# Kernel optimization log

Hardware: AMD Instinct MI355X
Metric: run time of the kernel (lower is better)

Reference implementation:

```python
import jax, jax.numpy as jnp
import numpy as np

N, E, H, R = 16384, 262144, 256, 64
INV_SQRT_3 = 1.0 / np.sqrt(3.0)
INV_SQRT_H = 1.0 / np.sqrt(float(H))
INV_SQRT_2 = 1.0 / np.sqrt(2.0)


def ssilu(t):
    # ScaledSiLU: silu(x) / 0.6
    return jax.nn.silu(t) * (1.0 / 0.6)


def layernorm(x, g, b):
    m = jnp.mean(x, axis=-1, keepdims=True)
    v = jnp.var(x, axis=-1, keepdims=True)
    return (x - m) * jax.lax.rsqrt(v + 1e-5) * g + b


def gated_equivariant_block(x, v, Wv1, Wv2, Wu1, bu1, Wu2, bu2, out_ch):
    # x: [N, Cin], v: [N, 3, Cin]
    vec1 = jnp.linalg.norm(v @ Wv1, axis=-2)          # [N, Cin]
    vec2 = v @ Wv2                                     # [N, 3, out_ch]
    h = ssilu(jnp.concatenate([x, vec1], axis=-1) @ Wu1 + bu1) @ Wu2 + bu2
    xn, vn = h[..., :out_ch], h[..., out_ch:]
    return ssilu(xn), vn[:, None, :] * vec2


def setup_inputs() -> dict:
    key = jax.random.key(0)
    ks = iter(jax.random.split(key, 48))

    def w(shape, fan_in):
        return jax.random.normal(next(ks), shape, jnp.float32) / np.sqrt(float(fan_in))

    return {
        "x": jax.random.normal(next(ks), (N, H), jnp.float32),
        "vec": jax.random.normal(next(ks), (N, 3, H), jnp.float32),
        "edge_rbf": jax.random.uniform(next(ks), (E, R), jnp.float32),
        "edge_vector": jax.random.normal(next(ks), (E, 3), jnp.float32),
        # PaiNNMessage params
        "ln_g": jnp.ones((H,), jnp.float32), "ln_b": jnp.zeros((H,), jnp.float32),
        "W_x1": w((H, H), H), "b_x1": jnp.zeros((H,), jnp.float32),
        "W_x2": w((H, 3 * H), H), "b_x2": jnp.zeros((3 * H,), jnp.float32),
        "W_rbf": w((R, 3 * H), R), "b_rbf": jnp.zeros((3 * H,), jnp.float32),
        # PaiNNUpdate params
        "W_vp": w((H, 2 * H), H),
        "W_xv1": w((2 * H, H), 2 * H), "b_xv1": jnp.zeros((H,), jnp.float32),
        "W_xv2": w((H, 3 * H), H), "b_xv2": jnp.zeros((3 * H,), jnp.float32),
        # PaiNNOutput block 1 (H -> H//2)
        "o1_Wv1": w((H, H), H), "o1_Wv2": w((H, H // 2), H),
        "o1_Wu1": w((2 * H, H), 2 * H), "o1_bu1": jnp.zeros((H,), jnp.float32),
        "o1_Wu2": w((H, H), H), "o1_bu2": jnp.zeros((H,), jnp.float32),
        # PaiNNOutput block 2 (H//2 -> 1)
        "o2_Wv1": w((H // 2, H // 2), H // 2), "o2_Wv2": w((H // 2, 1), H // 2),
        "o2_Wu1": w((H, H // 2), H), "o2_bu1": jnp.zeros((H // 2,), jnp.float32),
        "o2_Wu2": w((H // 2, 2), H // 2), "o2_bu2": jnp.zeros((2,), jnp.float32),
        "edge_index": jax.random.randint(next(ks), (2, E), 0, N),
    }


def reference(x, vec, edge_rbf, edge_vector,
              ln_g, ln_b, W_x1, b_x1, W_x2, b_x2, W_rbf, b_rbf,
              W_vp, W_xv1, b_xv1, W_xv2, b_xv2,
              o1_Wv1, o1_Wv2, o1_Wu1, o1_bu1, o1_Wu2, o1_bu2,
              o2_Wv1, o2_Wv2, o2_Wu1, o2_bu1, o2_Wu2, o2_bu2,
              edge_index):
    src, dst = edge_index[0], edge_index[1]

    # ---- PaiNNMessage ----
    xh = ssilu(layernorm(x, ln_g, ln_b) @ W_x1 + b_x1) @ W_x2 + b_x2   # [N, 3H]
    rbfh = edge_rbf @ W_rbf + b_rbf                                     # [E, 3H]
    m = xh[src] * rbfh                                                  # gather + fuse
    m1, m2, m3 = m[:, :H], m[:, H:2 * H], m[:, 2 * H:]
    m2 = m2 * INV_SQRT_3
    vmsg = (vec[src] * m2[:, None, :] + m3[:, None, :] * edge_vector[:, :, None]) * INV_SQRT_H  # [E,3,H]
    dx = jax.ops.segment_sum(m1, dst, num_segments=N)
    dvec = jax.ops.segment_sum(vmsg, dst, num_segments=N)
    x = x + dx
    vec = vec + dvec

    # ---- PaiNNUpdate ----
    vp = vec @ W_vp                                    # [N, 3, 2H]
    vec1, vec2 = vp[..., :H], vp[..., H:]
    vec_dot = jnp.sum(vec1 * vec2, axis=1) * INV_SQRT_H            # [N, H]
    vnorm = jnp.sqrt(jnp.sum(vec2 * vec2, axis=-2) + 1e-8)          # [N, H]
    xvh = ssilu(jnp.concatenate([x, vnorm], axis=-1) @ W_xv1 + b_xv1) @ W_xv2 + b_xv2
    xv1, xv2, xv3 = xvh[:, :H], xvh[:, H:2 * H], xvh[:, 2 * H:]
    x = x + (xv1 + xv2 * vec_dot) * INV_SQRT_2
    vec = vec + xv3[:, None, :] * vec1

    # ---- PaiNNOutput ----
    x, vec = gated_equivariant_block(x, vec, o1_Wv1, o1_Wv2, o1_Wu1, o1_bu1, o1_Wu2, o1_bu2, H // 2)
    x, vec = gated_equivariant_block(x, vec, o2_Wv1, o2_Wv2, o2_Wu1, o2_bu1, o2_Wu2, o2_bu2, 1)
    return jnp.squeeze(vec, axis=-1)   # [N, 3]
```

## Files before the change

### kernel.cpp

```cpp
#include <hip/hip_runtime.h>
#include <math.h>

#define NN 16384
#define EE 262144
#define HH 256

#define INV_SQRT_3f 0.57735026918962576f
#define INV_SQRT_Hf 0.0625f
#define INV_SQRT_2f 0.70710678118654752f
#define SSILU_SCALE 1.6666666666666667f

typedef __attribute__((ext_vector_type(8))) short bf16x8;
typedef __attribute__((ext_vector_type(4))) float f32x4;

__device__ __forceinline__ float ssilu_f(float v) {
    return v * (1.0f / (1.0f + __expf(-v))) * SSILU_SCALE;
}
__device__ __forceinline__ float b2f(short s) {
    unsigned int u = ((unsigned int)(unsigned short)s) << 16;
    return __uint_as_float(u);
}
__device__ __forceinline__ short f2b(float f) {
    unsigned int u = __float_as_uint(f);
    unsigned int r = (u + 0x7fff + ((u >> 16) & 1)) >> 16;
    return (short)r;
}

__global__ void __launch_bounds__(256) ln_kernel(const float* __restrict__ x,
                                                 const float* __restrict__ g,
                                                 const float* __restrict__ b,
                                                 short* __restrict__ oh,
                                                 short* __restrict__ ol) {
    int n = blockIdx.x;
    int t = threadIdx.x;
    float v = x[(long)n * HH + t];
    float s = v, s2 = v * v;
    #pragma unroll
    for (int off = 32; off > 0; off >>= 1) {
        s  += __shfl_down(s, off);
        s2 += __shfl_down(s2, off);
    }
    __shared__ float red[8];
    int wave = t >> 6, lane = t & 63;
    if (lane == 0) { red[wave] = s; red[4 + wave] = s2; }
    __syncthreads();
    __shared__ float mr[2];
    if (t == 0) {
        float ts = red[0] + red[1] + red[2] + red[3];
        float ts2 = red[4] + red[5] + red[6] + red[7];
        float mean = ts * (1.0f / HH);
        float var = ts2 * (1.0f / HH) - mean * mean;
        mr[0] = mean;
        mr[1] = rsqrtf(var + 1e-5f);
    }
    __syncthreads();
    float o = (v - mr[0]) * mr[1] * g[t] + b[t];
    short hh = f2b(o);
    oh[(long)n * HH + t] = hh;
    ol[(long)n * HH + t] = f2b(o - b2f(hh));
}

struct WtArgs {
    const float* W[11];
    int K[11];
    int N[11];
    int off[12];
};

__global__ void __launch_bounds__(256) wt_split_all(WtArgs a,
                                                    short* __restrict__ WTh,
                                                    short* __restrict__ WTl) {
    int idx = blockIdx.x * 256 + threadIdx.x;
    int s = 0;
    #pragma unroll
    for (int i = 1; i < 11; i++) s += (idx >= a.off[i]) ? 1 : 0;
    int local = idx - a.off[s];
    int K = a.K[s], N = a.N[s];
    int k = local / N, n = local - k * N;
    float w = a.W[s][local];
    short hh = f2b(w);
    long o = (long)a.off[s] + (long)n * K + k;
    WTh[o] = hh;
    WTl[o] = f2b(w - b2f(hh));
}

__global__ void __launch_bounds__(256) split4_kernel(const float* __restrict__ in,
                                                     short* __restrict__ h,
                                                     short* __restrict__ l) {
    long i = ((long)blockIdx.x * 256 + threadIdx.x) * 4;
    float4 v = *(const float4*)(in + i);
    short4 oh, ol;
    oh.x = f2b(v.x); ol.x = f2b(v.x - b2f(oh.x));
    oh.y = f2b(v.y); ol.y = f2b(v.y - b2f(oh.y));
    oh.z = f2b(v.z); ol.z = f2b(v.z - b2f(oh.z));
    oh.w = f2b(v.w); ol.w = f2b(v.w - b2f(oh.w));
    *(short4*)(h + i) = oh;
    *(short4*)(l + i) = ol;
}

__global__ void __launch_bounds__(256) mfma_gemm(const short* __restrict__ Ah,
                                                 const short* __restrict__ Al,
                                                 const short* __restrict__ Wh,
                                                 const short* __restrict__ Wl,
                                                 const float* __restrict__ bias,
                                                 void* __restrict__ Ch,
                                                 short* __restrict__ Cl,
                                                 int M, int K, int N, int act) {
    int tid = threadIdx.x;
    int wave = tid >> 6, lane = tid & 63;
    int quad = lane >> 4, l16 = lane & 15;
    long bm = (long)blockIdx.x * 128 + wave * 32;
    long bn = (long)blockIdx.y * 64;
    long a0 = (bm + l16) * K + quad * 8;
    long a1 = a0 + (long)16 * K;
    long w0 = (bn + l16) * K + quad * 8;

    f32x4 acc[2][4];
    #pragma unroll
    for (int f = 0; f < 2; f++)
        #pragma unroll
        for (int t = 0; t < 4; t++) acc[f][t] = (f32x4){0.f, 0.f, 0.f, 0.f};

    bf16x8 cah[2], cal[2], cbh[4], cbl[4];
    cah[0] = *(const bf16x8*)(Ah + a0);
    cah[1] = *(const bf16x8*)(Ah + a1);
    cal[0] = *(const bf16x8*)(Al + a0);
    cal[1] = *(const bf16x8*)(Al + a1);
    #pragma unroll
    for (int t = 0; t < 4; t++) {
        long wo = w0 + (long)t * 16 * K;
        cbh[t] = *(const bf16x8*)(Wh + wo);
        cbl[t] = *(const bf16x8*)(Wl + wo);
    }

    for (int k0 = 0; k0 < K; k0 += 32) {
        int k1 = k0 + 32;
        bf16x8 nah[2], nal[2], nbh[4], nbl[4];
        if (k1 < K) {
            nah[0] = *(const bf16x8*)(Ah + a0 + k1);
            nah[1] = *(const bf16x8*)(Ah + a1 + k1);
            nal[0] = *(const bf16x8*)(Al + a0 + k1);
            nal[1] = *(const bf16x8*)(Al + a1 + k1);
            #pragma unroll
            for (int t = 0; t < 4; t++) {
                long wo = w0 + (long)t * 16 * K + k1;
                nbh[t] = *(const bf16x8*)(Wh + wo);
                nbl[t] = *(const bf16x8*)(Wl + wo);
            }
        }
        #pragma unroll
        for (int t = 0; t < 4; t++) {
            #pragma unroll
            for (int f = 0; f < 2; f++) {
                acc[f][t] = __builtin_amdgcn_mfma_f32_16x16x32_bf16(cah[f], cbh[t], acc[f][t], 0, 0, 0);
                acc[f][t] = __builtin_amdgcn_mfma_f32_16x16x32_bf16(cal[f], cbh[t], acc[f][t], 0, 0, 0);
                acc[f][t] = __builtin_amdgcn_mfma_f32_16x16x32_bf16(cah[f], cbl[t], acc[f][t], 0, 0, 0);
            }
        }
        if (k1 < K) {
            cah[0] = nah[0]; cah[1] = nah[1];
            cal[0] = nal[0]; cal[1] = nal[1];
            #pragma unroll
            for (int t = 0; t < 4; t++) { cbh[t] = nbh[t]; cbl[t] = nbl[t]; }
        }
    }

    #pragma unroll
    for (int f = 0; f < 2; f++) {
        long row0 = bm + f * 16 + quad * 4;
        #pragma unroll
        for (int t = 0; t < 4; t++) {
            long col = bn + t * 16 + l16;
            float bv = bias ? bias[col] : 0.f;
            #pragma unroll
            for (int r = 0; r < 4; r++) {
                float v = acc[f][t][r] + bv;
                if (act & 1) v = ssilu_f(v);
                long idx = (row0 + r) * N + col;
                if (Cl) {
                    short hh = f2b(v);
                    ((short*)Ch)[idx] = hh;
                    Cl[idx] = f2b(v - b2f(hh));
                } else if (act & 2) {
                    ((short*)Ch)[idx] = f2b(v);
                } else {
                    ((float*)Ch)[idx] = v;
                }
            }
        }
    }
}

__global__ void __launch_bounds__(256) zero_kernel(int* __restrict__ p, int n) {
    int i = blockIdx.x * 256 + threadIdx.x;
    if (i < n) p[i] = 0;
}

__global__ void __launch_bounds__(256) hist_kernel(const int* __restrict__ eidx,
                                                   int* __restrict__ cnt) {
    int e = blockIdx.x * 256 + threadIdx.x;
    atomicAdd(&cnt[eidx[EE + e]], 1);
}

__global__ void __launch_bounds__(256) scan_kernel(int* __restrict__ cursor,
                                                   int* __restrict__ rowptr) {
    int t = threadIdx.x;
    int base_i = t * 64;
    int tsum = 0;
    for (int i = 0; i < 64; i++) tsum += cursor[base_i + i];
    __shared__ int ls[256];
    ls[t] = tsum;
    __syncthreads();
    for (int off = 1; off < 256; off <<= 1) {
        int v = (t >= off) ? ls[t - off] : 0;
        __syncthreads();
        ls[t] += v;
        __syncthreads();
    }
    int running = ls[t] - tsum;
    for (int i = 0; i < 64; i++) {
        int c = cursor[base_i + i];
        rowptr[base_i + i] = running;
        cursor[base_i + i] = running;
        running += c;
    }
    if (t == 255) rowptr[NN] = running;
}

__global__ void __launch_bounds__(256) scatter_kernel(const int* __restrict__ eidx,
                                                      int* __restrict__ cursor,
                                                      int* __restrict__ perm) {
    int e = blockIdx.x * 256 + threadIdx.x;
    int d_ = eidx[EE + e];
    int pos = atomicAdd(&cursor[d_], 1);
    perm[pos] = e;
}

__global__ void __launch_bounds__(256) deg_hist_kernel(const int* __restrict__ rowptr,
                                                       int* __restrict__ dhist) {
    int n = blockIdx.x * 256 + threadIdx.x;
    int deg = rowptr[n + 1] - rowptr[n];
    atomicAdd(&dhist[min(deg, 63)], 1);
}

__global__ void __launch_bounds__(64) deg_scan_kernel(int* __restrict__ dhist) {
    if (threadIdx.x == 0) {
        int run = 0;
        for (int b = 63; b >= 0; b--) {
            int c = dhist[b];
            dhist[b] = run;
            run += c;
        }
    }
}

__global__ void __launch_bounds__(256) deg_scatter_kernel(const int* __restrict__ rowptr,
                                                          int* __restrict__ dhist,
                                                          int* __restrict__ nodeorder) {
    int n = blockIdx.x * 256 + threadIdx.x;
    int deg = min(rowptr[n + 1] - rowptr[n], 63);
    int pos = atomicAdd(&dhist[deg], 1);
    nodeorder[pos] = n;
}

#define EPB 16

template <int NE>
__device__ __forceinline__ void rbf_gemm(const float* __restrict__ W_rbf, int t,
                                         const float (&rbf_s)[EPB][64],
                                         float bb1, float bb2, float bb3,
                                         float* __restrict__ acc1,
                                         float* __restrict__ acc2,
                                         float* __restrict__ acc3) {
    #pragma unroll
    for (int e = 0; e < NE; e++) { acc1[e] = bb1; acc2[e] = bb2; acc3[e] = bb3; }
    for (int k = 0; k < 64; k++) {
        float w1 = W_rbf[k * 768 + t];
        float w2 = W_rbf[k * 768 + 256 + t];
        float w3 = W_rbf[k * 768 + 512 + t];
        #pragma unroll
        for (int e = 0; e < NE; e++) {
            float r = rbf_s[e][k];
            acc1[e] += r * w1;
            acc2[e] += r * w2;
            acc3[e] += r * w3;
        }
    }
}

__global__ void __launch_bounds__(256) node_gather_kernel(
        const float* __restrict__ rbf,
        const float* __restrict__ W_rbf,
        const float* __restrict__ b_rbf,
        const float* __restrict__ xh,
        const float* __restrict__ vec,
        const float* __restrict__ ev,
        const int* __restrict__ eidx,
        const float* __restrict__ x,
        const int* __restrict__ perm,
        const int* __restrict__ rowptr,
        const int* __restrict__ nodeorder,
        float* __restrict__ x1,
        float* __restrict__ vecacc,
        short* __restrict__ vah,
        short* __restrict__ val) {
    int n = nodeorder[blockIdx.x];
    int t = threadIdx.x;
    int beg = rowptr[n], deg = rowptr[n + 1] - beg;

    __shared__ float rbf_s[EPB][64];
    __shared__ int eid_s[EPB], src_s[EPB];
    __shared__ float ev_s[EPB][3];

    float bb1 = b_rbf[t], bb2 = b_rbf[256 + t], bb3 = b_rbf[512 + t];
    float dxa = 0.f, dv0 = 0.f, dv1 = 0.f, dv2 = 0.f;
    float acc1[EPB], acc2[EPB], acc3[EPB];

    for (int b0 = 0; b0 < deg; b0 += EPB) {
        int cnt = min(EPB, deg - b0);
        __syncthreads();
        if (t < cnt) {
            int eid = perm[beg + b0 + t];
            eid_s[t] = eid;
            src_s[t] = eidx[eid];
        }
        __syncthreads();
        #pragma unroll
        for (int i = 0; i < (EPB * 64) / 256; i++) {
            int idx = i * 256 + t;
            int e = idx >> 6, k = idx & 63;
            rbf_s[e][k] = (e < cnt) ? rbf[(long)eid_s[e] * 64 + k] : 0.f;
        }
        if (t < cnt * 3) {
            int e = t / 3, d = t % 3;
            ev_s[e][d] = ev[(long)eid_s[e] * 3 + d];
        }
        __syncthreads();

        if (cnt > 8)      rbf_gemm<16>(W_rbf, t, rbf_s, bb1, bb2, bb3, acc1, acc2, acc3);
        else if (cnt > 4) rbf_gemm<8>(W_rbf, t, rbf_s, bb1, bb2, bb3, acc1, acc2, acc3);
        else              rbf_gemm<4>(W_rbf, t, rbf_s, bb1, bb2, bb3, acc1, acc2, acc3);

        #define EDGE_ACC(e)                                                   \
            {                                                                 \
                int s = src_s[e];                                             \
                const float* xr = xh + (long)s * 768;                         \
                const float* vr = vec + (long)s * 768;                        \
                float m1 = acc1[e] * xr[t];                                   \
                float m2 = acc2[e] * xr[256 + t] * INV_SQRT_3f;               \
                float m3 = acc3[e] * xr[512 + t];                             \
                dxa += m1;                                                    \
                dv0 += (vr[t] * m2       + m3 * ev_s[e][0]) * INV_SQRT_Hf;    \
                dv1 += (vr[256 + t] * m2 + m3 * ev_s[e][1]) * INV_SQRT_Hf;    \
                dv2 += (vr[512 + t] * m2 + m3 * ev_s[e][2]) * INV_SQRT_Hf;    \
            }

        if (cnt == EPB) {
            #pragma unroll 4
            for (int e = 0; e < EPB; e++) EDGE_ACC(e)
        } else {
            for (int e = 0; e < cnt; e++) EDGE_ACC(e)
        }
        #undef EDGE_ACC
    }

    long nb = (long)n * 256 + t;
    x1[nb] = x[nb] + dxa;
    long vb = (long)n * 768 + t;
    float vv0 = vec[vb] + dv0;
    float vv1 = vec[vb + 256] + dv1;
    float vv2 = vec[vb + 512] + dv2;
    vecacc[vb]       = vv0;
    vecacc[vb + 256] = vv1;
    vecacc[vb + 512] = vv2;
    short h0 = f2b(vv0), h1 = f2b(vv1), h2 = f2b(vv2);
    vah[vb]       = h0;  val[vb]       = f2b(vv0 - b2f(h0));
    vah[vb + 256] = h1;  val[vb + 256] = f2b(vv1 - b2f(h1));
    vah[vb + 512] = h2;  val[vb + 512] = f2b(vv2 - b2f(h2));
}

__global__ void __launch_bounds__(256) vdot_cat_kernel(const float* __restrict__ vec1,
                                                       const short* __restrict__ vec2,
                                                       const float* __restrict__ x1,
                                                       float* __restrict__ vdot,
                                                       short* __restrict__ cath,
                                                       short* __restrict__ catl) {
    int idx = blockIdx.x * 256 + threadIdx.x;
    int n = idx >> 8, h = idx & 255;
    float dsum = 0.f, s2 = 0.f;
    #pragma unroll
    for (int d = 0; d < 3; d++) {
        long r = (long)(n * 3 + d) * 256 + h;
        float a = vec1[r];
        float b = b2f(vec2[r]);
        dsum += a * b;
        s2 += b * b;
    }
    vdot[idx] = dsum * INV_SQRT_Hf;
    float xv = x1[idx];
    short hh = f2b(xv);
    cath[(long)n * 512 + h] = hh;
    catl[(long)n * 512 + h] = f2b(xv - b2f(hh));
    float vn = sqrtf(s2 + 1e-8f);
    short vh = f2b(vn);
    cath[(long)n * 512 + 256 + h] = vh;
    catl[(long)n * 512 + 256 + h] = f2b(vn - b2f(vh));
}

__global__ void __launch_bounds__(256) e4_kernel(float* __restrict__ x1,
                                                 float* __restrict__ vecacc,
                                                 const float* __restrict__ vec1,
                                                 const float* __restrict__ vdot,
                                                 const short* __restrict__ xvh_h,
                                                 const short* __restrict__ xvh_l) {
    int idx = blockIdx.x * 256 + threadIdx.x;
    int n = idx >> 8, h = idx & 255;
    long b0 = (long)n * 768 + h;
    float xv1 = b2f(xvh_h[b0])       + b2f(xvh_l[b0]);
    float xv2 = b2f(xvh_h[b0 + 256]) + b2f(xvh_l[b0 + 256]);
    float xv3 = b2f(xvh_h[b0 + 512]) + b2f(xvh_l[b0 + 512]);
    x1[idx] = x1[idx] + (xv1 + xv2 * vdot[idx]) * INV_SQRT_2f;
    #pragma unroll
    for (int d = 0; d < 3; d++) {
        long r = (long)(n * 3 + d) * 256 + h;
        vecacc[r] = vecacc[r] + xv3 * vec1[r];
    }
}

__global__ void __launch_bounds__(256) normcat_kernel(const float* __restrict__ xin,
                                                      const short* __restrict__ w,
                                                      short* __restrict__ cath,
                                                      short* __restrict__ catl,
                                                      int Cx, int C, int shift) {
    int idx = blockIdx.x * 256 + threadIdx.x;
    int cols = 1 << shift;
    int n = idx >> shift, c = idx & (cols - 1);
    float v;
    if (c < Cx) {
        v = xin[(long)n * Cx + c];
    } else {
        int cc = c - Cx;
        float s = 0.f;
        #pragma unroll
        for (int d = 0; d < 3; d++) {
            float a = b2f(w[(long)(n * 3 + d) * C + cc]);
            s += a * a;
        }
        v = sqrtf(s);
    }
    short hh = f2b(v);
    cath[idx] = hh;
    catl[idx] = f2b(v - b2f(hh));
}

__global__ void __launch_bounds__(256) gate1_kernel(const float* __restrict__ h1,
                                                    const short* __restrict__ w2h,
                                                    const short* __restrict__ w2l,
                                                    float* __restrict__ x3,
                                                    short* __restrict__ vecCh,
                                                    short* __restrict__ vecCl) {
    int idx = blockIdx.x * 256 + threadIdx.x;
    int n = idx >> 7, c = idx & 127;
    x3[idx] = ssilu_f(h1[(long)n * 256 + c]);
    float vn = h1[(long)n * 256 + 128 + c];
    #pragma unroll
    for (int d = 0; d < 3; d++) {
        long r = (long)(n * 3 + d) * 128 + c;
        float wv = b2f(w2h[r]) + b2f(w2l[r]);
        float v = vn * wv;
        short hh = f2b(v);
        vecCh[r] = hh;
        vecCl[r] = f2b(v - b2f(hh));
    }
}

__global__ void __launch_bounds__(256) g12_kernel(const short* __restrict__ vecCh,
                                                  const short* __restrict__ vecCl,
                                                  const float* __restrict__ Wv2,
                                                  float* __restrict__ w4) {
    int row = blockIdx.x * 4 + (threadIdx.x >> 6);
    int lane = threadIdx.x & 63;
    long r0 = (long)row * 128 + lane;
    float v0 = b2f(vecCh[r0]) + b2f(vecCl[r0]);
    float v1 = b2f(vecCh[r0 + 64]) + b2f(vecCl[r0 + 64]);
    float s = v0 * Wv2[lane] + v1 * Wv2[64 + lane];
    #pragma unroll
    for (int off = 32; off > 0; off >>= 1) s += __shfl_down(s, off);
    if (lane == 0) w4[row] = s;
}

__global__ void __launch_bounds__(256) final_kernel(const float* __restrict__ t5,
                                                    const float* __restrict__ Wu2,
                                                    const float* __restrict__ bu2,
                                                    const float* __restrict__ w4,
                                                    float* __restrict__ out) {
    int n = blockIdx.x * 4 + (threadIdx.x >> 6);
    int lane = threadIdx.x & 63;
    float s = t5[(long)n * 128 + lane] * Wu2[lane * 2 + 1] +
              t5[(long)n * 128 + 64 + lane] * Wu2[(64 + lane) * 2 + 1];
    #pragma unroll
    for (int off = 32; off > 0; off >>= 1) s += __shfl_down(s, off);
    float val = __shfl(s, 0) + bu2[1];
    if (lane < 3) out[(long)n * 3 + lane] = val * w4[(long)n * 3 + lane];
}

extern "C" void kernel_launch(void* const* d_in, const int* in_sizes, int n_in,
                              void* d_out, int out_size, void* d_ws, size_t ws_size,
                              hipStream_t stream) {
    const float* x          = (const float*)d_in[0];
    const float* vec        = (const float*)d_in[1];
    const float* edge_rbf   = (const float*)d_in[2];
    const float* edge_vector= (const float*)d_in[3];
    const float* ln_g       = (const float*)d_in[4];
    const float* ln_b       = (const float*)d_in[5];
    const float* W_x1       = (const float*)d_in[6];
    const float* b_x1       = (const float*)d_in[7];
    const float* W_x2       = (const float*)d_in[8];
    const float* b_x2       = (const float*)d_in[9];
    const float* W_rbf      = (const float*)d_in[10];
    const float* b_rbf      = (const float*)d_in[11];
    const float* W_vp       = (const float*)d_in[12];
    const float* W_xv1      = (const float*)d_in[13];
    const float* b_xv1      = (const float*)d_in[14];
    const float* W_xv2      = (const float*)d_in[15];
    const float* b_xv2      = (const float*)d_in[16];
    const float* o1_Wv1     = (const float*)d_in[17];
    const float* o1_Wv2     = (const float*)d_in[18];
    const float* o1_Wu1     = (const float*)d_in[19];
    const float* o1_bu1     = (const float*)d_in[20];
    const float* o1_Wu2     = (const float*)d_in[21];
    const float* o1_bu2     = (const float*)d_in[22];
    const float* o2_Wv1     = (const float*)d_in[23];
    const float* o2_Wv2     = (const float*)d_in[24];
    const float* o2_Wu1     = (const float*)d_in[25];
    const float* o2_bu1     = (const float*)d_in[26];
    const float* o2_Wu2     = (const float*)d_in[27];
    const float* o2_bu2     = (const float*)d_in[28];
    const int*   edge_index = (const int*)d_in[29];
    float* out = (float*)d_out;
    float* ws  = (float*)d_ws;

    const size_t S = (size_t)NN * 256;
    const size_t Q = S / 4;
    float* x1      = ws;
    float* vecacc  = ws + 4 * Q;
    short* wtb     = (short*)(ws + 16 * Q);
    const long WLO = 1064960;
    short* xln_h = (short*)(ws + 18 * Q);
    short* xln_l = (short*)(ws + 20 * Q);
    short* t1_h  = (short*)(ws + 22 * Q);
    short* t1_l  = (short*)(ws + 24 * Q);
    float* xh    = ws + 30 * Q;
    int* rowptr    = (int*)(ws + 48 * Q);
    int* cursor    = rowptr + (NN + 1);
    int* dhist     = cursor + NN;
    int* nodeorder = dhist + 64;
    int* perm      = nodeorder + NN;
    short* vah   = (short*)(ws + 18 * Q);
    short* val_  = (short*)(ws + 24 * Q);
    float* vec1  = ws + 30 * Q;
    short* vec2b = (short*)(ws + 42 * Q);
    float* vdot  = ws + 48 * Q;
    short* catb_h = (short*)(ws + 18 * Q);
    short* catb_l = (short*)(ws + 22 * Q);
    short* t2_h  = (short*)(ws + 26 * Q);
    short* t2_l  = (short*)(ws + 28 * Q);
    short* xvh_h = (short*)(ws + 18 * Q);
    short* xvh_l = (short*)(ws + 42 * Q);
    short* vah2  = (short*)(ws + 18 * Q);
    short* val2  = (short*)(ws + 24 * Q);
    short* w1b   = (short*)(ws + 30 * Q);
    short* w2_h  = (short*)(ws + 36 * Q);
    short* w2_l  = (short*)(ws + 39 * Q);
    short* cat2_h = (short*)(ws + 42 * Q);
    short* cat2_l = (short*)(ws + 46 * Q);
    short* t4_h  = (short*)(ws + 18 * Q);
    short* t4_l  = (short*)(ws + 20 * Q);
    float* h1    = ws + 22 * Q;
    float* x3    = ws + 26 * Q;
    short* vecC_h = (short*)(ws + 28 * Q);
    short* vecC_l = (short*)(ws + 31 * Q);
    short* w3b   = (short*)(ws + 34 * Q);
    float* w4    = ws + 37 * Q;
    short* cat3_h = (short*)(ws + 38 * Q);
    short* cat3_l = (short*)(ws + 40 * Q);
    float* t5    = ws + 42 * Q;

    short* WT_x1    = wtb;
    short* WT_x2    = wtb + 65536;
    short* WT_vp    = wtb + 262144;
    short* WT_xv1   = wtb + 393216;
    short* WT_xv2   = wtb + 524288;
    short* WT_o1Wv1 = wtb + 720896;
    short* WT_o1Wv2 = wtb + 786432;
    short* WT_o1Wu1 = wtb + 819200;
    short* WT_o1Wu2 = wtb + 950272;
    short* WT_o2Wv1 = wtb + 1015808;
    short* WT_o2Wu1 = wtb + 1032192;

    WtArgs wa;
    const float* wsrc[11] = {W_x1, W_x2, W_vp, W_xv1, W_xv2, o1_Wv1, o1_Wv2,
                             o1_Wu1, o1_Wu2, o2_Wv1, o2_Wu1};
    int wk[11] = {256, 256, 256, 512, 256, 256, 256, 512, 256, 128, 256};
    int wn[11] = {256, 768, 512, 256, 768, 256, 128, 256, 256, 128, 128};
    int off = 0;
    for (int i = 0; i < 11; i++) {
        wa.W[i] = wsrc[i]; wa.K[i] = wk[i]; wa.N[i] = wn[i];
        wa.off[i] = off; off += wk[i] * wn[i];
    }
    wa.off[11] = off;
    wt_split_all<<<off / 256, 256, 0, stream>>>(wa, wtb, wtb + WLO);

    ln_kernel<<<NN, 256, 0, stream>>>(x, ln_g, ln_b, xln_h, xln_l);
    mfma_gemm<<<dim3(NN / 128, 4), 256, 0, stream>>>(xln_h, xln_l, WT_x1, WT_x1 + WLO,
                                                     b_x1, t1_h, t1_l, NN, 256, 256, 1);
    mfma_gemm<<<dim3(NN / 128, 12), 256, 0, stream>>>(t1_h, t1_l, WT_x2, WT_x2 + WLO,
                                                      b_x2, xh, nullptr, NN, 256, 768, 0);

    zero_kernel<<<(NN + 64 + 255) / 256, 256, 0, stream>>>(cursor, NN + 64);
    hist_kernel<<<EE / 256, 256, 0, stream>>>(edge_index, cursor);
    scan_kernel<<<1, 256, 0, stream>>>(cursor, rowptr);
    scatter_kernel<<<EE / 256, 256, 0, stream>>>(edge_index, cursor, perm);
    deg_hist_kernel<<<NN / 256, 256, 0, stream>>>(rowptr, dhist);
    deg_scan_kernel<<<1, 64, 0, stream>>>(dhist);
    deg_scatter_kernel<<<NN / 256, 256, 0, stream>>>(rowptr, dhist, nodeorder);
    node_gather_kernel<<<NN, 256, 0, stream>>>(edge_rbf, W_rbf, b_rbf, xh, vec,
                                               edge_vector, edge_index, x,
                                               perm, rowptr, nodeorder, x1, vecacc,
                                               vah, val_);

    mfma_gemm<<<dim3(3 * NN / 128, 4), 256, 0, stream>>>(vah, val_, WT_vp, WT_vp + WLO,
                                                         nullptr, vec1, nullptr,
                                                         3 * NN, 256, 256, 0);
    mfma_gemm<<<dim3(3 * NN / 128, 4), 256, 0, stream>>>(vah, val_, WT_vp + 65536,
                                                         WT_vp + WLO + 65536,
                                                         nullptr, vec2b, nullptr,
                                                         3 * NN, 256, 256, 2);
    vdot_cat_kernel<<<NN, 256, 0, stream>>>(vec1, vec2b, x1, vdot, catb_h, catb_l);
    mfma_gemm<<<dim3(NN / 128, 4), 256, 0, stream>>>(catb_h, catb_l, WT_xv1, WT_xv1 + WLO,
                                                     b_xv1, t2_h, t2_l, NN, 512, 256, 1);
    mfma_gemm<<<dim3(NN / 128, 12), 256, 0, stream>>>(t2_h, t2_l, WT_xv2, WT_xv2 + WLO,
                                                      b_xv2, xvh_h, xvh_l, NN, 256, 768, 0);
    e4_kernel<<<NN, 256, 0, stream>>>(x1, vecacc, vec1, vdot, xvh_h, xvh_l);

    split4_kernel<<<3 * S / 1024, 256, 0, stream>>>(vecacc, vah2, val2);
    mfma_gemm<<<dim3(3 * NN / 128, 4), 256, 0, stream>>>(vah2, val2, WT_o1Wv1, WT_o1Wv1 + WLO,
                                                         nullptr, w1b, nullptr,
                                                         3 * NN, 256, 256, 2);
    mfma_gemm<<<dim3(3 * NN / 128, 2), 256, 0, stream>>>(vah2, val2, WT_o1Wv2, WT_o1Wv2 + WLO,
                                                         nullptr, w2_h, w2_l,
                                                         3 * NN, 256, 128, 0);
    normcat_kernel<<<NN * 512 / 256, 256, 0, stream>>>(x1, w1b, cat2_h, cat2_l, 256, 256, 9);
    mfma_gemm<<<dim3(NN / 128, 4), 256, 0, stream>>>(cat2_h, cat2_l, WT_o1Wu1, WT_o1Wu1 + WLO,
                                                     o1_bu1, t4_h, t4_l, NN, 512, 256, 1);
    mfma_gemm<<<dim3(NN / 128, 4), 256, 0, stream>>>(t4_h, t4_l, WT_o1Wu2, WT_o1Wu2 + WLO,
                                                     o1_bu2, h1, nullptr, NN, 256, 256, 0);
    gate1_kernel<<<NN * 128 / 256, 256, 0, stream>>>(h1, w2_h, w2_l, x3, vecC_h, vecC_l);

    mfma_gemm<<<dim3(3 * NN / 128, 2), 256, 0, stream>>>(vecC_h, vecC_l, WT_o2Wv1,
                                                         WT_o2Wv1 + WLO, nullptr,
                                                         w3b, nullptr, 3 * NN, 128, 128, 2);
    g12_kernel<<<3 * NN / 4, 256, 0, stream>>>(vecC_h, vecC_l, o2_Wv2, w4);
    normcat_kernel<<<NN * 256 / 256, 256, 0, stream>>>(x3, w3b, cat3_h, cat3_l, 128, 128, 8);
    mfma_gemm<<<dim3(NN / 128, 2), 256, 0, stream>>>(cat3_h, cat3_l, WT_o2Wu1, WT_o2Wu1 + WLO,
                                                     o2_bu1, t5, nullptr, NN, 256, 128, 1);
    final_kernel<<<NN / 4, 256, 0, stream>>>(t5, o2_Wu2, o2_bu2, w4, out);
}
```

Before: 1.678 ms.

## Compute per-edge RBF projection with split-bf16 MFMA inside node gather kernel

Replaces the scalar FP32 RBF-to-filter GEMM in the node gather kernel with 16x16x32 bf16 MFMA instructions, using a hi/lo bf16 split (three MFMAs per step) so accuracy stays close to fp32. W_rbf is added to the transposed weight-split preprocessing, and the RBF tile is split into hi/lo bf16 in shared memory. MFMA results are staged through a shared buffer and consumed one output slice at a time. This trades the per-thread FMA loop and its register arrays for extra syncs and shared-memory traffic, and it computes all 16 edge rows even when a node has fewer edges.

```diff
diff --git a/kernel.cpp b/kernel.cpp
--- a/kernel.cpp
+++ b/kernel.cpp
@@ -61,10 +61,10 @@
 }
 
 struct WtArgs {
-    const float* W[11];
-    int K[11];
-    int N[11];
-    int off[12];
+    const float* W[12];
+    int K[12];
+    int N[12];
+    int off[13];
 };
 
 __global__ void __launch_bounds__(256) wt_split_all(WtArgs a,
@@ -73,7 +73,7 @@
     int idx = blockIdx.x * 256 + threadIdx.x;
     int s = 0;
     #pragma unroll
-    for (int i = 1; i < 11; i++) s += (idx >= a.off[i]) ? 1 : 0;
+    for (int i = 1; i < 12; i++) s += (idx >= a.off[i]) ? 1 : 0;
     int local = idx - a.off[s];
     int K = a.K[s], N = a.N[s];
     int k = local / N, n = local - k * N;
@@ -265,32 +265,10 @@
 
 #define EPB 16
 
-template <int NE>
-__device__ __forceinline__ void rbf_gemm(const float* __restrict__ W_rbf, int t,
-                                         const float (&rbf_s)[EPB][64],
-                                         float bb1, float bb2, float bb3,
-                                         float* __restrict__ acc1,
-                                         float* __restrict__ acc2,
-                                         float* __restrict__ acc3) {
-    #pragma unroll
-    for (int e = 0; e < NE; e++) { acc1[e] = bb1; acc2[e] = bb2; acc3[e] = bb3; }
-    for (int k = 0; k < 64; k++) {
-        float w1 = W_rbf[k * 768 + t];
-        float w2 = W_rbf[k * 768 + 256 + t];
-        float w3 = W_rbf[k * 768 + 512 + t];
-        #pragma unroll
-        for (int e = 0; e < NE; e++) {
-            float r = rbf_s[e][k];
-            acc1[e] += r * w1;
-            acc2[e] += r * w2;
-            acc3[e] += r * w3;
-        }
-    }
-}
-
 __global__ void __launch_bounds__(256) node_gather_kernel(
         const float* __restrict__ rbf,
-        const float* __restrict__ W_rbf,
+        const short* __restrict__ Wrh,
+        const short* __restrict__ Wrl,
         const float* __restrict__ b_rbf,
         const float* __restrict__ xh,
         const float* __restrict__ vec,
@@ -306,15 +284,24 @@
         short* __restrict__ val) {
     int n = nodeorder[blockIdx.x];
     int t = threadIdx.x;
+    int wave = t >> 6, lane = t & 63;
+    int quad = lane >> 4, l16 = lane & 15;
     int beg = rowptr[n], deg = rowptr[n + 1] - beg;
 
-    __shared__ float rbf_s[EPB][64];
+    __shared__ __align__(16) short ah_s[EPB][72];
+    __shared__ __align__(16) short al_s[EPB][72];
+    __shared__ float mm[EPB][265];
     __shared__ int eid_s[EPB], src_s[EPB];
     __shared__ float ev_s[EPB][3];
 
-    float bb1 = b_rbf[t], bb2 = b_rbf[256 + t], bb3 = b_rbf[512 + t];
     float dxa = 0.f, dv0 = 0.f, dv1 = 0.f, dv2 = 0.f;
-    float acc1[EPB], acc2[EPB], acc3[EPB];
+
+    float bb[3][4];
+    #pragma unroll
+    for (int s = 0; s < 3; s++)
+        #pragma unroll
+        for (int tt = 0; tt < 4; tt++)
+            bb[s][tt] = b_rbf[s * 256 + wave * 64 + tt * 16 + l16];
 
     for (int b0 = 0; b0 < deg; b0 += EPB) {
         int cnt = min(EPB, deg - b0);
@@ -329,39 +316,73 @@
         for (int i = 0; i < (EPB * 64) / 256; i++) {
             int idx = i * 256 + t;
             int e = idx >> 6, k = idx & 63;
-            rbf_s[e][k] = (e < cnt) ? rbf[(long)eid_s[e] * 64 + k] : 0.f;
+            float r = (e < cnt) ? rbf[(long)eid_s[e] * 64 + k] : 0.f;
+            short hh = f2b(r);
+            ah_s[e][k] = hh;
+            al_s[e][k] = f2b(r - b2f(hh));
         }
         if (t < cnt * 3) {
             int e = t / 3, d = t % 3;
             ev_s[e][d] = ev[(long)eid_s[e] * 3 + d];
         }
         __syncthreads();
-
-        if (cnt > 8)      rbf_gemm<16>(W_rbf, t, rbf_s, bb1, bb2, bb3, acc1, acc2, acc3);
-        else if (cnt > 4) rbf_gemm<8>(W_rbf, t, rbf_s, bb1, bb2, bb3, acc1, acc2, acc3);
-        else              rbf_gemm<4>(W_rbf, t, rbf_s, bb1, bb2, bb3, acc1, acc2, acc3);
-
-        #define EDGE_ACC(e)                                                   \
-            {                                                                 \
-                int s = src_s[e];                                             \
-                const float* xr = xh + (long)s * 768;                         \
-                const float* vr = vec + (long)s * 768;                        \
-                float m1 = acc1[e] * xr[t];                                   \
-                float m2 = acc2[e] * xr[256 + t] * INV_SQRT_3f;               \
-                float m3 = acc3[e] * xr[512 + t];                             \
-                dxa += m1;                                                    \
-                dv0 += (vr[t] * m2       + m3 * ev_s[e][0]) * INV_SQRT_Hf;    \
-                dv1 += (vr[256 + t] * m2 + m3 * ev_s[e][1]) * INV_SQRT_Hf;    \
-                dv2 += (vr[512 + t] * m2 + m3 * ev_s[e][2]) * INV_SQRT_Hf;    \
+        bf16x8 afh[2], afl[2];
+        #pragma unroll
+        for (int ks = 0; ks < 2; ks++) {
+            afh[ks] = *(const bf16x8*)(&ah_s[l16][ks * 32 + quad * 8]);
+            afl[ks] = *(const bf16x8*)(&al_s[l16][ks * 32 + quad * 8]);
+        }
+
+        #pragma unroll
+        for (int s = 0; s < 3; s++) {
+            f32x4 acc[4];
+            #pragma unroll
+            for (int tt = 0; tt < 4; tt++) {
+                int col = s * 256 + wave * 64 + tt * 16 + l16;
+                float bv = bb[s][tt];
+                acc[tt] = (f32x4){bv, bv, bv, bv};
+                #pragma unroll
+                for (int ks = 0; ks < 2; ks++) {
+                    bf16x8 bh = *(const bf16x8*)(Wrh + (long)col * 64 + ks * 32 + quad * 8);
+                    bf16x8 bl = *(const bf16x8*)(Wrl + (long)col * 64 + ks * 32 + quad * 8);
+                    acc[tt] = __builtin_amdgcn_mfma_f32_16x16x32_bf16(afh[ks], bh, acc[tt], 0, 0, 0);
+                    acc[tt] = __builtin_amdgcn_mfma_f32_16x16x32_bf16(afl[ks], bh, acc[tt], 0, 0, 0);
+                    acc[tt] = __builtin_amdgcn_mfma_f32_16x16x32_bf16(afh[ks], bl, acc[tt], 0, 0, 0);
+                }
             }
-
-        if (cnt == EPB) {
-            #pragma unroll 4
-            for (int e = 0; e < EPB; e++) EDGE_ACC(e)
-        } else {
-            for (int e = 0; e < cnt; e++) EDGE_ACC(e)
-        }
-        #undef EDGE_ACC
+            __syncthreads();
+            #pragma unroll
+            for (int tt = 0; tt < 4; tt++) {
+                #pragma unroll
+                for (int r = 0; r < 4; r++)
+                    mm[quad * 4 + r][wave * 64 + tt * 16 + l16] = acc[tt][r];
+            }
+            __syncthreads();
+            if (s == 0) {
+                for (int e = 0; e < cnt; e++) {
+                    int sr = src_s[e];
+                    dxa += mm[e][t] * xh[(long)sr * 768 + t];
+                }
+            } else if (s == 1) {
+                for (int e = 0; e < cnt; e++) {
+                    int sr = src_s[e];
+                    float m2 = mm[e][t] * xh[(long)sr * 768 + 256 + t] *
+                               (INV_SQRT_3f * INV_SQRT_Hf);
+                    const float* vr = vec + (long)sr * 768;
+                    dv0 += vr[t] * m2;
+                    dv1 += vr[256 + t] * m2;
+                    dv2 += vr[512 + t] * m2;
+                }
+            } else {
+                for (int e = 0; e < cnt; e++) {
+                    int sr = src_s[e];
+                    float m3 = mm[e][t] * xh[(long)sr * 768 + 512 + t] * INV_SQRT_Hf;
+                    dv0 += m3 * ev_s[e][0];
+                    dv1 += m3 * ev_s[e][1];
+                    dv2 += m3 * ev_s[e][2];
+                }
+            }
+        }
     }
 
     long nb = (long)n * 256 + t;
@@ -545,7 +566,7 @@
     float* x1      = ws;
     float* vecacc  = ws + 4 * Q;
     short* wtb     = (short*)(ws + 16 * Q);
-    const long WLO = 1064960;
+    const long WLO = 1114112;
     short* xln_h = (short*)(ws + 18 * Q);
     short* xln_l = (short*)(ws + 20 * Q);
     short* t1_h  = (short*)(ws + 22 * Q);
@@ -597,18 +618,19 @@
     short* WT_o1Wu2 = wtb + 950272;
     short* WT_o2Wv1 = wtb + 1015808;
     short* WT_o2Wu1 = wtb + 1032192;
+    short* WT_rbf   = wtb + 1064960;
 
     WtArgs wa;
-    const float* wsrc[11] = {W_x1, W_x2, W_vp, W_xv1, W_xv2, o1_Wv1, o1_Wv2,
-                             o1_Wu1, o1_Wu2, o2_Wv1, o2_Wu1};
-    int wk[11] = {256, 256, 256, 512, 256, 256, 256, 512, 256, 128, 256};
-    int wn[11] = {256, 768, 512, 256, 768, 256, 128, 256, 256, 128, 128};
+    const float* wsrc[12] = {W_x1, W_x2, W_vp, W_xv1, W_xv2, o1_Wv1, o1_Wv2,
+                             o1_Wu1, o1_Wu2, o2_Wv1, o2_Wu1, W_rbf};
+    int wk[12] = {256, 256, 256, 512, 256, 256, 256, 512, 256, 128, 256, 64};
+    int wn[12] = {256, 768, 512, 256, 768, 256, 128, 256, 256, 128, 128, 768};
     int off = 0;
-    for (int i = 0; i < 11; i++) {
+    for (int i = 0; i < 12; i++) {
         wa.W[i] = wsrc[i]; wa.K[i] = wk[i]; wa.N[i] = wn[i];
         wa.off[i] = off; off += wk[i] * wn[i];
     }
-    wa.off[11] = off;
+    wa.off[12] = off;
     wt_split_all<<<off / 256, 256, 0, stream>>>(wa, wtb, wtb + WLO);
 
     ln_kernel<<<NN, 256, 0, stream>>>(x, ln_g, ln_b, xln_h, xln_l);
@@ -624,9 +646,9 @@
     deg_hist_kernel<<<NN / 256, 256, 0, stream>>>(rowptr, dhist);
     deg_scan_kernel<<<1, 64, 0, stream>>>(dhist);
     deg_scatter_kernel<<<NN / 256, 256, 0, stream>>>(rowptr, dhist, nodeorder);
-    node_gather_kernel<<<NN, 256, 0, stream>>>(edge_rbf, W_rbf, b_rbf, xh, vec,
-                                               edge_vector, edge_index, x,
-                                               perm, rowptr, nodeorder, x1, vecacc,
+    node_gather_kernel<<<NN, 256, 0, stream>>>(edge_rbf, WT_rbf, WT_rbf + WLO,
+                                               b_rbf, xh, vec, edge_vector, edge_index,
+                                               x, perm, rowptr, nodeorder, x1, vecacc,
                                                vah, val_);
 
     mfma_gemm<<<dim3(3 * NN / 128, 4), 256, 0, stream>>>(vah, val_, WT_vp, WT_vp + WLO,
```

Measured after the change: 2.643 ms. 1.57x slower.
